# Optimization experiments

Measured on AMD Instinct MI355X. Metric: run time of the kernel, lower is better.

Reference implementation:

```python
import jax, jax.numpy as jnp
import numpy as np

SHIFT, REDUCE = 3, 2
B, L, E, H = 64, 512, 300, 256


def _make_transitions():
    # Left-branching valid parse: S S R S R S R ... (L shifts, L-1 reduces)
    T = 2 * L - 1
    tr = np.full(T, REDUCE, dtype=np.int64)
    tr[0] = SHIFT
    tr[1::2] = SHIFT
    return jnp.asarray(np.tile(tr[None, :], (B, 1)))


def setup_inputs() -> dict:
    key = jax.random.key(0)
    ks = jax.random.split(key, 5)
    s = 0.05
    return {
        "sentence": jax.random.normal(ks[0], (B, L, E), jnp.float32),
        "transitions": _make_transitions(),
        "W_word": jax.random.normal(ks[1], (E, 2 * H), jnp.float32) * s,
        "b_word": jnp.zeros((2 * H,), jnp.float32),
        "W_left": jax.random.normal(ks[2], (H, 5 * H), jnp.float32) * s,
        "W_right": jax.random.normal(ks[3], (H, 5 * H), jnp.float32) * s,
        "b_reduce": jnp.zeros((5 * H,), jnp.float32),
    }


def reference(sentence, transitions, W_word, b_word, W_left, W_right, b_reduce):
    Bsz, Ls, _ = sentence.shape
    Hs = W_left.shape[0]
    proj = sentence @ W_word + b_word                  # [B, L, 2H] (word projection; BN/dropout disabled)
    h_buf, c_buf = jnp.split(proj, 2, axis=2)          # buffers, each [B, L, H]
    T = transitions.shape[1]
    bidx = jnp.arange(Bsz)

    def step(carry, trans_t):
        sh, sc, ptr, bp = carry                        # thin stacks [B,T+2,H], pointers [B]
        shift = trans_t == SHIFT
        i1 = jnp.maximum(ptr - 1, 0)                   # right child (stack top)
        i2 = jnp.maximum(ptr - 2, 0)                   # left child
        hl, cl = sh[bidx, i2], sc[bidx, i2]
        hr, cr = sh[bidx, i1], sc[bidx, i1]
        g = hl @ W_left + hr @ W_right + b_reduce      # [B, 5H] TreeLSTM gates
        ig, flg, frg, og, ug = jnp.split(g, 5, axis=1)
        c_red = (jax.nn.sigmoid(flg) * cl + jax.nn.sigmoid(frg) * cr
                 + jax.nn.sigmoid(ig) * jnp.tanh(ug))
        h_red = jax.nn.sigmoid(og) * jnp.tanh(c_red)
        bsafe = jnp.minimum(bp, Ls - 1)
        val_h = jnp.where(shift[:, None], h_buf[bidx, bsafe], h_red)
        val_c = jnp.where(shift[:, None], c_buf[bidx, bsafe], c_red)
        pos = jnp.where(shift, ptr, i2)                # shift pushes at ptr; reduce writes at ptr-2
        sh = sh.at[bidx, pos].set(val_h)
        sc = sc.at[bidx, pos].set(val_c)
        ptr = ptr + jnp.where(shift, 1, -1)
        bp = bp + shift.astype(bp.dtype)
        return (sh, sc, ptr, bp), None

    sh0 = jnp.zeros((Bsz, T + 2, Hs), sentence.dtype)
    sc0 = jnp.zeros((Bsz, T + 2, Hs), sentence.dtype)
    ptr0 = jnp.zeros((Bsz,), jnp.int32)
    bp0 = jnp.zeros((Bsz,), jnp.int32)
    (sh, sc, ptr, _), _ = jax.lax.scan(
        step, (sh0, sc0, ptr0, bp0), jnp.swapaxes(transitions, 0, 1))
    return sh[bidx, jnp.maximum(ptr - 1, 0)]           # final stack top h: [B, H]
```

## Files before the change

### kernel.cpp

```cpp
#include <hip/hip_runtime.h>
#include <hip/hip_bf16.h>
#include <math.h>

#define BSZ   64
#define LSEQ  512
#define EDIM  300
#define HDIM  256
#define TLEN  1023
#define PROJW 512
#define GW    1280

#define NROW  8
#define NHID  8
#define RGBLK 32
#define NRG   8
#define NBLK  256
#define SLOTS 2

#define PROJ_N   (BSZ*LSEQ*PROJW)
#define STACKF   PROJ_N
#define STACK_N  (2*BSZ*SLOTS*2*HDIM)
#define FLAG_OFF (STACKF + STACK_N)
#define FLAGS_N  1024
#define ARR_OFF  (FLAG_OFF + FLAGS_N)
#define ARR_STRIDE 16

#define NODEBIT 0x80000000u
#define SENT    0xFFFFFFFFu
#define LROW    264
#define HRO     (NROW*LROW + 4)
#define RPITCH  328
#define RROW    41

__global__ void __launch_bounds__(256)
proj_gemm(const float* __restrict__ A, const float* __restrict__ W,
          const float* __restrict__ bias, float* __restrict__ out) {
    __shared__ float As[8][65];
    __shared__ float Bs[8][64];
    const int tid = threadIdx.x;
    const int tx = tid & 15, ty = tid >> 4;
    const int bm = blockIdx.y, bn = blockIdx.x;

    float acc[4][4] = {};
    const int e  = tid * 2;
    const int ar = e >> 3, ac = e & 7;
    const int br = e >> 6, bc = e & 63;

    for (int k0 = 0; k0 < EDIM; k0 += 8) {
        __syncthreads();
        {
            const float* Ap = A + (size_t)(bm * 64 + ar) * EDIM;
            int gk = k0 + ac;
            As[ac][ar]     = (gk     < EDIM) ? Ap[gk]     : 0.f;
            As[ac + 1][ar] = (gk + 1 < EDIM) ? Ap[gk + 1] : 0.f;
            int gkb = k0 + br;
            float w0 = 0.f, w1 = 0.f;
            if (gkb < EDIM) {
                const float* Wp = W + (size_t)gkb * PROJW + bn * 64;
                w0 = Wp[bc]; w1 = Wp[bc + 1];
            }
            Bs[br][bc] = w0; Bs[br][bc + 1] = w1;
        }
        __syncthreads();
        #pragma unroll
        for (int kk = 0; kk < 8; ++kk) {
            float a[4], b[4];
            #pragma unroll
            for (int i = 0; i < 4; ++i) a[i] = As[kk][ty * 4 + i];
            #pragma unroll
            for (int j = 0; j < 4; ++j) b[j] = Bs[kk][tx * 4 + j];
            #pragma unroll
            for (int i = 0; i < 4; ++i)
                #pragma unroll
                for (int j = 0; j < 4; ++j)
                    acc[i][j] += a[i] * b[j];
        }
    }
    #pragma unroll
    for (int i = 0; i < 4; ++i) {
        const int row  = bm * 64 + ty * 4 + i;
        const int col0 = bn * 64 + tx * 4;
        float* op = out + (size_t)row * PROJW + col0;
        #pragma unroll
        for (int j = 0; j < 4; ++j) op[j] = acc[i][j] + bias[col0 + j];
    }
}

__global__ void flags_kernel(const int* __restrict__ trans, int* __restrict__ flags) {
    const int t = blockIdx.x * 256 + threadIdx.x;
    if (t >= TLEN) return;
    int f = 0;
    for (int b = 0; b < BSZ; ++b) f |= (trans[(size_t)b * TLEN + t] != 3) ? 1 : 0;
    flags[t] = f;
}

__device__ __forceinline__ unsigned encodeH(short tag, int slot, int grow) {
    if (tag >= 0)  return (unsigned)(((size_t)grow * LSEQ + (int)tag) * PROJW);
    if (tag <= -3) return SENT;
    const int par = (tag == -2) ? 1 : 0;
    return NODEBIT | (unsigned)(STACKF + ((par * BSZ + grow) * SLOTS + slot) * (2 * HDIM));
}

__device__ __forceinline__ float cohLoad(const float* ws, unsigned off) {
    return __uint_as_float(__hip_atomic_load((const unsigned*)ws + off,
                          __ATOMIC_RELAXED, __HIP_MEMORY_SCOPE_AGENT));
}
__device__ __forceinline__ float2 cohLoad2(const float* ws, unsigned off) {
    unsigned long long v = __hip_atomic_load((const unsigned long long*)(ws + off),
                          __ATOMIC_RELAXED, __HIP_MEMORY_SCOPE_AGENT);
    union { unsigned long long u; float2 f; } cv; cv.u = v;
    return cv.f;
}
__device__ __forceinline__ void cohStore(float* ws, unsigned off, float v) {
    __hip_atomic_store((unsigned*)ws + off, __float_as_uint(v),
                       __ATOMIC_RELAXED, __HIP_MEMORY_SCOPE_AGENT);
}

__device__ __forceinline__ float loadC(const float* ws, unsigned oh, int gn) {
    if (oh == SENT) return 0.f;
    if (oh & NODEBIT) return cohLoad(ws, (oh & ~NODEBIT) + HDIM + gn);
    return ws[oh + HDIM + gn];
}

__device__ __forceinline__ int qswz(int Q, int row) {
    return Q ^ row ^ ((Q >> 3) & 7);
}

__device__ __forceinline__ void stage_rows(float* __restrict__ buf,
    const unsigned* __restrict__ desc, const int* __restrict__ isred,
    const float* __restrict__ ws, int srow, int sc, bool nodePhase) {
    if (!isred[srow]) return;
    const unsigned oh = desc[srow];
    if (!nodePhase) {
        if (oh == SENT) {
            const float4 z = make_float4(0.f, 0.f, 0.f, 0.f);
            #pragma unroll
            for (int j = 0; j < 2; ++j) {
                const int Q = sc + 32 * j;
                *(float4*)&buf[srow * LROW + 4 * qswz(Q, srow)] = z;
            }
        } else if (!(oh & NODEBIT)) {
            const float4* s = (const float4*)(ws + oh);
            #pragma unroll
            for (int j = 0; j < 2; ++j) {
                const int Q = sc + 32 * j;
                *(float4*)&buf[srow * LROW + 4 * qswz(Q, srow)] = s[Q];
            }
        }
    } else if (oh != SENT && (oh & NODEBIT)) {
        const unsigned base = oh & ~NODEBIT;
        #pragma unroll
        for (int j = 0; j < 2; ++j) {
            const int Q = sc + 32 * j;
            const float2 lo = cohLoad2(ws, base + 4 * Q);
            const float2 hi = cohLoad2(ws, base + 4 * Q + 2);
            *(float4*)&buf[srow * LROW + 4 * qswz(Q, srow)] = make_float4(lo.x, lo.y, hi.x, hi.y);
        }
    }
}

__global__ void __launch_bounds__(256, 1)
scan_coop(const int* __restrict__ trans,
          const float* __restrict__ Wl, const float* __restrict__ Wr,
          const float* __restrict__ bred,
          float* __restrict__ ws, float* __restrict__ out) {
    __shared__ __align__(16) float hbuf[HRO + NROW * LROW];
    __shared__ __align__(16) float red[16 * RPITCH];
    __shared__ unsigned tbits[NROW][32];
    __shared__ unsigned fbits[32];
    __shared__ short    tg[NROW][SLOTS];
    __shared__ unsigned d_hl[NROW], d_hr[NROW], d_wr[NROW], d_oh[NROW];
    __shared__ int      isred[NROW];

    const int tid   = threadIdx.x;
    const int rg    = blockIdx.x & 7;
    const int cs    = blockIdx.x >> 3;
    const int rbase = rg * NROW;
    const int n0    = cs * NHID;

    const int srow = tid >> 5, sc = tid & 31;
    const int colq = tid & 7;
    const int rh   = (tid >> 3) & 1;
    const int m    = (tid >> 4) & 1;
    const int w8   = tid >> 5;
    const int gn   = n0 + colq;

    const int* flags  = (const int*)(ws + FLAG_OFF);
    unsigned*  arr    = (unsigned*)(ws + ARR_OFF);
    unsigned*  myslot = &arr[(size_t)blockIdx.x * ARR_STRIDE];

    float4 w[8][5];
    {
        const float* src = (m == 0) ? Wl : Wr;
        const int kbase = w8 * 32;
        #pragma unroll
        for (int j = 0; j < 8; ++j) {
            const int k0 = kbase + j * 4;
            #pragma unroll
            for (int g = 0; g < 5; ++g) {
                w[j][g].x = src[(size_t)(k0 + 0) * GW + g * HDIM + gn];
                w[j][g].y = src[(size_t)(k0 + 1) * GW + g * HDIM + gn];
                w[j][g].z = src[(size_t)(k0 + 2) * GW + g * HDIM + gn];
                w[j][g].w = src[(size_t)(k0 + 3) * GW + g * HDIM + gn];
            }
        }
    }
    #pragma unroll
    for (int j = 0; j < 8; ++j)
        #pragma unroll
        for (int g = 0; g < 5; ++g)
            asm volatile("" : "+v"(w[j][g].x), "+v"(w[j][g].y),
                              "+v"(w[j][g].z), "+v"(w[j][g].w));

    if (tid < NROW * 32) {
        const int r2 = tid >> 5, wd = tid & 31;
        unsigned bits = 0;
        for (int j = 0; j < 32; ++j) {
            const int t = wd * 32 + j;
            if (t < TLEN && trans[(size_t)(rbase + r2) * TLEN + t] == 3) bits |= (1u << j);
        }
        tbits[r2][wd] = bits;
    }
    if (tid < 32) {
        unsigned bits = 0;
        for (int j = 0; j < 32; ++j) {
            const int t = tid * 32 + j;
            if (t < TLEN && flags[t]) bits |= (1u << j);
        }
        fbits[tid] = bits;
    }
    if (tid < NROW) {
        tg[tid][0] = -3; tg[tid][1] = -3;
        isred[tid] = 0;
    }

    float bv[5];
    #pragma unroll
    for (int g = 0; g < 5; ++g) bv[g] = bred[g * HDIM + gn];

    int ptr = 0, bp = 0;
    unsigned nbar = 0;
    __syncthreads();

    for (int t = 0; t < TLEN; ++t) {
        if (tid < NROW) {
            const int r = tid, grow = rbase + r;
            const int is_shift = (tbits[r][t >> 5] >> (t & 31)) & 1;
            if (is_shift) {
                int pos = ptr; if (pos < 0) pos = 0; if (pos > SLOTS - 1) pos = SLOTS - 1;
                tg[r][pos] = (short)min(bp, LSEQ - 1);
                ptr++; bp++;
                isred[r] = 0;
            } else {
                const int i1 = min(max(ptr - 1, 0), SLOTS - 1);
                const int i2 = min(max(ptr - 2, 0), SLOTS - 1);
                const short t1 = tg[r][i1], t2 = tg[r][i2];
                d_hl[r] = encodeH(t2, i2, grow);
                d_hr[r] = encodeH(t1, i1, grow);
                const int pnew = (t2 == -1) ? 1 : 0;
                d_wr[r] = (unsigned)(STACKF + ((pnew * BSZ + grow) * SLOTS + i2) * (2 * HDIM));
                tg[r][i2] = (short)(pnew ? -2 : -1);
                ptr--;
                isred[r] = 1;
            }
        }
        __syncthreads();

        if (!((fbits[t >> 5] >> (t & 31)) & 1)) continue;
        ++nbar;

        stage_rows(hbuf,       d_hl, isred, ws, srow, sc, false);
        stage_rows(hbuf + HRO, d_hr, isred, ws, srow, sc, false);

        if (tid < RGBLK) {
            const unsigned* slot = &arr[(size_t)(tid * NRG + rg) * ARR_STRIDE];
            while (__hip_atomic_load(slot, __ATOMIC_RELAXED, __HIP_MEMORY_SCOPE_AGENT) < nbar - 1)
                __builtin_amdgcn_s_sleep(1);
        }
        __syncthreads();

        stage_rows(hbuf,       d_hl, isred, ws, srow, sc, true);
        stage_rows(hbuf + HRO, d_hr, isred, ws, srow, sc, true);
        __syncthreads();

        float cl = 0.f, cr = 0.f;
        if (tid < 64) {
            const int orow = tid >> 3;
            if (isred[orow]) {
                cl = loadC(ws, d_hl[orow], gn);
                cr = loadC(ws, d_hr[orow], gn);
            }
        }

        float acc[4][5];
        #pragma unroll
        for (int r = 0; r < 4; ++r)
            #pragma unroll
            for (int g = 0; g < 5; ++g) acc[r][g] = 0.f;

        {
            const float* hb = hbuf + m * HRO;
            #pragma unroll
            for (int j = 0; j < 8; ++j) {
                const int kq = w8 * 8 + j;
                #pragma unroll
                for (int r = 0; r < 4; ++r) {
                    const int row = rh * 4 + r;
                    const float4 x = *(const float4*)&hb[row * LROW + 4 * qswz(kq, row)];
                    #pragma unroll
                    for (int g = 0; g < 5; ++g)
                        acc[r][g] += x.x * w[j][g].x + x.y * w[j][g].y
                                   + x.z * w[j][g].z + x.w * w[j][g].w;
                }
            }
        }

        {
            const int g16 = w8 * 2 + m;
            #pragma unroll
            for (int r = 0; r < 4; ++r) {
                const int row = rh * 4 + r;
                #pragma unroll
                for (int g = 0; g < 5; ++g)
                    red[g16 * RPITCH + row * RROW + colq * 5 + g] = acc[r][g];
            }
        }
        __syncthreads();

        if (tid < 64) {
            const int orow = tid >> 3;
            if (isred[orow]) {
                float s[5];
                #pragma unroll
                for (int g = 0; g < 5; ++g) s[g] = bv[g];
                #pragma unroll
                for (int q = 0; q < 16; ++q)
                    #pragma unroll
                    for (int g = 0; g < 5; ++g)
                        s[g] += red[q * RPITCH + orow * RROW + colq * 5 + g];
                const float si = 1.f / (1.f + expf(-s[0]));
                const float sl = 1.f / (1.f + expf(-s[1]));
                const float sr = 1.f / (1.f + expf(-s[2]));
                const float so = 1.f / (1.f + expf(-s[3]));
                const float c_red = sl * cl + sr * cr + si * tanhf(s[4]);
                const float h_red = so * tanhf(c_red);
                cohStore(ws, d_wr[orow] + gn, h_red);
                cohStore(ws, d_wr[orow] + HDIM + gn, c_red);
            }
            asm volatile("s_waitcnt vmcnt(0)" ::: "memory");
            if (tid == 0)
                __hip_atomic_store(myslot, nbar, __ATOMIC_RELAXED, __HIP_MEMORY_SCOPE_AGENT);
        }
    }

    if (tid < RGBLK) {
        const unsigned* slot = &arr[(size_t)(tid * NRG + rg) * ARR_STRIDE];
        while (__hip_atomic_load(slot, __ATOMIC_RELAXED, __HIP_MEMORY_SCOPE_AGENT) < nbar)
            __builtin_amdgcn_s_sleep(1);
    }
    __syncthreads();
    if (tid < NROW) {
        const int top = min(max(ptr - 1, 0), SLOTS - 1);
        d_oh[tid] = encodeH(tg[tid][top], top, rbase + tid);
    }
    __syncthreads();
    if (tid < 64) {
        const int orow = tid >> 3;
        const unsigned oh = d_oh[orow];
        float v;
        if (oh == SENT) v = 0.f;
        else if (oh & NODEBIT) v = cohLoad(ws, (oh & ~NODEBIT) + gn);
        else v = ws[oh + gn];
        out[(size_t)(rbase + orow) * HDIM + gn] = v;
    }
}

extern "C" void kernel_launch(void* const* d_in, const int* in_sizes, int n_in,
                              void* d_out, int out_size, void* d_ws, size_t ws_size,
                              hipStream_t stream) {
    const float* sentence    = (const float*)d_in[0];
    const int*   transitions = (const int*)  d_in[1];
    const float* W_word      = (const float*)d_in[2];
    const float* b_word      = (const float*)d_in[3];
    const float* W_left      = (const float*)d_in[4];
    const float* W_right     = (const float*)d_in[5];
    const float* b_reduce    = (const float*)d_in[6];
    float* out  = (float*)d_out;
    float* ws_f = (float*)d_ws;

    hipMemsetAsync((char*)d_ws + (size_t)ARR_OFF * 4, 0,
                   (size_t)NBLK * ARR_STRIDE * 4, stream);

    flags_kernel<<<(TLEN + 255) / 256, 256, 0, stream>>>(
        transitions, (int*)(ws_f + FLAG_OFF));

    dim3 g1(PROJW / 64, (BSZ * LSEQ) / 64);
    proj_gemm<<<g1, 256, 0, stream>>>(sentence, W_word, b_word, ws_f);

    scan_coop<<<NBLK, 256, 0, stream>>>(transitions, W_left, W_right, b_reduce,
                                        ws_f, out);
}
```

Before: 2.849 ms.

## Replace per-step block barrier with epoch-tagged h values and local c stack

Removes the per-step cross-block flag barrier. Each reduced h value is now stored as a 64-bit word whose upper half holds the step epoch, so consumers spin only on the exact data they need instead of on 32 producer block flags. Cell states c stay in shared memory, because each block owns its own hidden columns, so they no longer round-trip through global memory. The reduce-step flags are now derived in-kernel from the transition bits of the block's own 8 rows, which drops the flags kernel. This narrows synchronization to true data dependencies, at the cost of wider atomic loads and spin-polling per element.

```diff
diff --git a/kernel.cpp b/kernel.cpp
--- a/kernel.cpp
+++ b/kernel.cpp
@@ -12,18 +12,15 @@
 
 #define NROW  8
 #define NHID  8
-#define RGBLK 32
 #define NRG   8
 #define NBLK  256
 #define SLOTS 2
 
 #define PROJ_N   (BSZ*LSEQ*PROJW)
 #define STACKF   PROJ_N
-#define STACK_N  (2*BSZ*SLOTS*2*HDIM)
-#define FLAG_OFF (STACKF + STACK_N)
-#define FLAGS_N  1024
-#define ARR_OFF  (FLAG_OFF + FLAGS_N)
-#define ARR_STRIDE 16
+#define PAIRB    (STACKF/2)
+#define PAIR_N   (2*BSZ*SLOTS*HDIM)
+#define PAIR_CNT (2*BSZ*SLOTS*HDIM)
 
 #define NODEBIT 0x80000000u
 #define SENT    0xFFFFFFFFu
@@ -86,77 +83,8 @@
     }
 }
 
-__global__ void flags_kernel(const int* __restrict__ trans, int* __restrict__ flags) {
-    const int t = blockIdx.x * 256 + threadIdx.x;
-    if (t >= TLEN) return;
-    int f = 0;
-    for (int b = 0; b < BSZ; ++b) f |= (trans[(size_t)b * TLEN + t] != 3) ? 1 : 0;
-    flags[t] = f;
-}
-
-__device__ __forceinline__ unsigned encodeH(short tag, int slot, int grow) {
-    if (tag >= 0)  return (unsigned)(((size_t)grow * LSEQ + (int)tag) * PROJW);
-    if (tag <= -3) return SENT;
-    const int par = (tag == -2) ? 1 : 0;
-    return NODEBIT | (unsigned)(STACKF + ((par * BSZ + grow) * SLOTS + slot) * (2 * HDIM));
-}
-
-__device__ __forceinline__ float cohLoad(const float* ws, unsigned off) {
-    return __uint_as_float(__hip_atomic_load((const unsigned*)ws + off,
-                          __ATOMIC_RELAXED, __HIP_MEMORY_SCOPE_AGENT));
-}
-__device__ __forceinline__ float2 cohLoad2(const float* ws, unsigned off) {
-    unsigned long long v = __hip_atomic_load((const unsigned long long*)(ws + off),
-                          __ATOMIC_RELAXED, __HIP_MEMORY_SCOPE_AGENT);
-    union { unsigned long long u; float2 f; } cv; cv.u = v;
-    return cv.f;
-}
-__device__ __forceinline__ void cohStore(float* ws, unsigned off, float v) {
-    __hip_atomic_store((unsigned*)ws + off, __float_as_uint(v),
-                       __ATOMIC_RELAXED, __HIP_MEMORY_SCOPE_AGENT);
-}
-
-__device__ __forceinline__ float loadC(const float* ws, unsigned oh, int gn) {
-    if (oh == SENT) return 0.f;
-    if (oh & NODEBIT) return cohLoad(ws, (oh & ~NODEBIT) + HDIM + gn);
-    return ws[oh + HDIM + gn];
-}
-
 __device__ __forceinline__ int qswz(int Q, int row) {
     return Q ^ row ^ ((Q >> 3) & 7);
-}
-
-__device__ __forceinline__ void stage_rows(float* __restrict__ buf,
-    const unsigned* __restrict__ desc, const int* __restrict__ isred,
-    const float* __restrict__ ws, int srow, int sc, bool nodePhase) {
-    if (!isred[srow]) return;
-    const unsigned oh = desc[srow];
-    if (!nodePhase) {
-        if (oh == SENT) {
-            const float4 z = make_float4(0.f, 0.f, 0.f, 0.f);
-            #pragma unroll
-            for (int j = 0; j < 2; ++j) {
-                const int Q = sc + 32 * j;
-                *(float4*)&buf[srow * LROW + 4 * qswz(Q, srow)] = z;
-            }
-        } else if (!(oh & NODEBIT)) {
-            const float4* s = (const float4*)(ws + oh);
-            #pragma unroll
-            for (int j = 0; j < 2; ++j) {
-                const int Q = sc + 32 * j;
-                *(float4*)&buf[srow * LROW + 4 * qswz(Q, srow)] = s[Q];
-            }
-        }
-    } else if (oh != SENT && (oh & NODEBIT)) {
-        const unsigned base = oh & ~NODEBIT;
-        #pragma unroll
-        for (int j = 0; j < 2; ++j) {
-            const int Q = sc + 32 * j;
-            const float2 lo = cohLoad2(ws, base + 4 * Q);
-            const float2 hi = cohLoad2(ws, base + 4 * Q + 2);
-            *(float4*)&buf[srow * LROW + 4 * qswz(Q, srow)] = make_float4(lo.x, lo.y, hi.x, hi.y);
-        }
-    }
 }
 
 __global__ void __launch_bounds__(256, 1)
@@ -166,10 +94,15 @@
           float* __restrict__ ws, float* __restrict__ out) {
     __shared__ __align__(16) float hbuf[HRO + NROW * LROW];
     __shared__ __align__(16) float red[16 * RPITCH];
+    __shared__ float    cstk[2 * SLOTS * NROW * NHID];
     __shared__ unsigned tbits[NROW][32];
     __shared__ unsigned fbits[32];
     __shared__ short    tg[NROW][SLOTS];
-    __shared__ unsigned d_hl[NROW], d_hr[NROW], d_wr[NROW], d_oh[NROW];
+    __shared__ unsigned eps[NROW][SLOTS];
+    __shared__ unsigned d_hl[NROW], d_hr[NROW], d_wr[NROW];
+    __shared__ unsigned e_hl[NROW], e_hr[NROW];
+    __shared__ unsigned c_l[NROW], c_r[NROW], cw[NROW];
+    __shared__ unsigned d_oh[NROW], e_oh[NROW];
     __shared__ int      isred[NROW];
 
     const int tid   = threadIdx.x;
@@ -184,10 +117,9 @@
     const int m    = (tid >> 4) & 1;
     const int w8   = tid >> 5;
     const int gn   = n0 + colq;
-
-    const int* flags  = (const int*)(ws + FLAG_OFF);
-    unsigned*  arr    = (unsigned*)(ws + ARR_OFF);
-    unsigned*  myslot = &arr[(size_t)blockIdx.x * ARR_STRIDE];
+    const int orow = tid >> 3;
+
+    unsigned long long* p64 = (unsigned long long*)ws;
 
     float4 w[8][5];
     {
@@ -221,17 +153,18 @@
         }
         tbits[r2][wd] = bits;
     }
-    if (tid < 32) {
-        unsigned bits = 0;
-        for (int j = 0; j < 32; ++j) {
-            const int t = tid * 32 + j;
-            if (t < TLEN && flags[t]) bits |= (1u << j);
-        }
-        fbits[tid] = bits;
-    }
     if (tid < NROW) {
         tg[tid][0] = -3; tg[tid][1] = -3;
+        eps[tid][0] = 0; eps[tid][1] = 0;
         isred[tid] = 0;
+    }
+    __syncthreads();
+    if (tid < 32) {
+        unsigned fb = 0;
+        #pragma unroll
+        for (int r2 = 0; r2 < NROW; ++r2) fb |= ~tbits[r2][tid];
+        if (tid == 31) fb &= 0x7FFFFFFFu;
+        fbits[tid] = fb;
     }
 
     float bv[5];
@@ -243,6 +176,9 @@
     __syncthreads();
 
     for (int t = 0; t < TLEN; ++t) {
+        const int redstep = (fbits[t >> 5] >> (t & 31)) & 1;
+        if (redstep) ++nbar;
+
         if (tid < NROW) {
             const int r = tid, grow = rbase + r;
             const int is_shift = (tbits[r][t >> 5] >> (t & 31)) & 1;
@@ -255,10 +191,26 @@
                 const int i1 = min(max(ptr - 1, 0), SLOTS - 1);
                 const int i2 = min(max(ptr - 2, 0), SLOTS - 1);
                 const short t1 = tg[r][i1], t2 = tg[r][i2];
-                d_hl[r] = encodeH(t2, i2, grow);
-                d_hr[r] = encodeH(t1, i1, grow);
+                unsigned dl, el = 0, cdl;
+                if (t2 >= 0)       { dl = (unsigned)((grow * LSEQ + (int)t2) * PROJW); cdl = dl + HDIM; }
+                else if (t2 <= -3) { dl = SENT; cdl = SENT; }
+                else { const int par = (t2 == -2);
+                       dl = NODEBIT | (unsigned)(PAIRB + ((par * BSZ + grow) * SLOTS + i2) * HDIM);
+                       el = eps[r][i2];
+                       cdl = NODEBIT | (unsigned)(par * 2 + i2); }
+                unsigned dr, er = 0, cdr;
+                if (t1 >= 0)       { dr = (unsigned)((grow * LSEQ + (int)t1) * PROJW); cdr = dr + HDIM; }
+                else if (t1 <= -3) { dr = SENT; cdr = SENT; }
+                else { const int par = (t1 == -2);
+                       dr = NODEBIT | (unsigned)(PAIRB + ((par * BSZ + grow) * SLOTS + i1) * HDIM);
+                       er = eps[r][i1];
+                       cdr = NODEBIT | (unsigned)(par * 2 + i1); }
+                d_hl[r] = dl; e_hl[r] = el; c_l[r] = cdl;
+                d_hr[r] = dr; e_hr[r] = er; c_r[r] = cdr;
                 const int pnew = (t2 == -1) ? 1 : 0;
-                d_wr[r] = (unsigned)(STACKF + ((pnew * BSZ + grow) * SLOTS + i2) * (2 * HDIM));
+                d_wr[r] = (unsigned)(PAIRB + ((pnew * BSZ + grow) * SLOTS + i2) * HDIM);
+                cw[r]   = (unsigned)(pnew * 2 + i2);
+                eps[r][i2] = nbar;
                 tg[r][i2] = (short)(pnew ? -2 : -1);
                 ptr--;
                 isred[r] = 1;
@@ -266,30 +218,54 @@
         }
         __syncthreads();
 
-        if (!((fbits[t >> 5] >> (t & 31)) & 1)) continue;
-        ++nbar;
-
-        stage_rows(hbuf,       d_hl, isred, ws, srow, sc, false);
-        stage_rows(hbuf + HRO, d_hr, isred, ws, srow, sc, false);
-
-        if (tid < RGBLK) {
-            const unsigned* slot = &arr[(size_t)(tid * NRG + rg) * ARR_STRIDE];
-            while (__hip_atomic_load(slot, __ATOMIC_RELAXED, __HIP_MEMORY_SCOPE_AGENT) < nbar - 1)
-                __builtin_amdgcn_s_sleep(1);
-        }
-        __syncthreads();
-
-        stage_rows(hbuf,       d_hl, isred, ws, srow, sc, true);
-        stage_rows(hbuf + HRO, d_hr, isred, ws, srow, sc, true);
-        __syncthreads();
-
-        float cl = 0.f, cr = 0.f;
-        if (tid < 64) {
-            const int orow = tid >> 3;
-            if (isred[orow]) {
-                cl = loadC(ws, d_hl[orow], gn);
-                cr = loadC(ws, d_hr[orow], gn);
-            }
+        if (!redstep) continue;
+
+        if (isred[srow]) {
+            #pragma unroll
+            for (int buf = 0; buf < 2; ++buf) {
+                float* hb = hbuf + buf * HRO;
+                const unsigned oh = buf ? d_hr[srow] : d_hl[srow];
+                const unsigned ee = buf ? e_hr[srow] : e_hl[srow];
+                float h[8];
+                if (oh == SENT) {
+                    #pragma unroll
+                    for (int i = 0; i < 8; ++i) h[i] = 0.f;
+                } else if (!(oh & NODEBIT)) {
+                    const float4 a = *(const float4*)(ws + oh + sc * 8);
+                    const float4 b = *(const float4*)(ws + oh + sc * 8 + 4);
+                    h[0]=a.x; h[1]=a.y; h[2]=a.z; h[3]=a.w;
+                    h[4]=b.x; h[5]=b.y; h[6]=b.z; h[7]=b.w;
+                } else {
+                    const unsigned pb = (oh & ~NODEBIT) + sc * 8;
+                    unsigned long long v[8];
+                    for (;;) {
+                        #pragma unroll
+                        for (int i = 0; i < 8; ++i)
+                            v[i] = __hip_atomic_load(p64 + pb + i,
+                                     __ATOMIC_RELAXED, __HIP_MEMORY_SCOPE_AGENT);
+                        bool ok = true;
+                        #pragma unroll
+                        for (int i = 0; i < 8; ++i)
+                            ok &= ((unsigned)(v[i] >> 32) >= ee);
+                        if (ok) break;
+                        __builtin_amdgcn_s_sleep(1);
+                    }
+                    #pragma unroll
+                    for (int i = 0; i < 8; ++i) h[i] = __uint_as_float((unsigned)v[i]);
+                }
+                *(float4*)&hb[srow * LROW + 4 * qswz(2 * sc + 0, srow)] =
+                    make_float4(h[0], h[1], h[2], h[3]);
+                *(float4*)&hb[srow * LROW + 4 * qswz(2 * sc + 1, srow)] =
+                    make_float4(h[4], h[5], h[6], h[7]);
+            }
+        }
+        __syncthreads();
+
+        float clw = 0.f, crw = 0.f;
+        if (tid < 64 && isred[orow]) {
+            const unsigned cdl = c_l[orow], cdr = c_r[orow];
+            if (cdl != SENT && !(cdl & NODEBIT)) clw = ws[cdl + gn];
+            if (cdr != SENT && !(cdr & NODEBIT)) crw = ws[cdr + gn];
         }
 
         float acc[4][5];
@@ -297,7 +273,6 @@
         for (int r = 0; r < 4; ++r)
             #pragma unroll
             for (int g = 0; g < 5; ++g) acc[r][g] = 0.f;
-
         {
             const float* hb = hbuf + m * HRO;
             #pragma unroll
@@ -314,7 +289,6 @@
                 }
             }
         }
-
         {
             const int g16 = w8 * 2 + m;
             #pragma unroll
@@ -328,7 +302,6 @@
         __syncthreads();
 
         if (tid < 64) {
-            const int orow = tid >> 3;
             if (isred[orow]) {
                 float s[5];
                 #pragma unroll
@@ -338,39 +311,53 @@
                     #pragma unroll
                     for (int g = 0; g < 5; ++g)
                         s[g] += red[q * RPITCH + orow * RROW + colq * 5 + g];
+                const unsigned cdl = c_l[orow], cdr = c_r[orow];
+                const float cl = (cdl == SENT) ? 0.f :
+                    ((cdl & NODEBIT) ? cstk[((cdl & 3) * NROW + orow) * NHID + colq] : clw);
+                const float cr = (cdr == SENT) ? 0.f :
+                    ((cdr & NODEBIT) ? cstk[((cdr & 3) * NROW + orow) * NHID + colq] : crw);
                 const float si = 1.f / (1.f + expf(-s[0]));
                 const float sl = 1.f / (1.f + expf(-s[1]));
                 const float sr = 1.f / (1.f + expf(-s[2]));
                 const float so = 1.f / (1.f + expf(-s[3]));
                 const float c_red = sl * cl + sr * cr + si * tanhf(s[4]);
                 const float h_red = so * tanhf(c_red);
-                cohStore(ws, d_wr[orow] + gn, h_red);
-                cohStore(ws, d_wr[orow] + HDIM + gn, c_red);
-            }
-            asm volatile("s_waitcnt vmcnt(0)" ::: "memory");
-            if (tid == 0)
-                __hip_atomic_store(myslot, nbar, __ATOMIC_RELAXED, __HIP_MEMORY_SCOPE_AGENT);
-        }
-    }
-
-    if (tid < RGBLK) {
-        const unsigned* slot = &arr[(size_t)(tid * NRG + rg) * ARR_STRIDE];
-        while (__hip_atomic_load(slot, __ATOMIC_RELAXED, __HIP_MEMORY_SCOPE_AGENT) < nbar)
-            __builtin_amdgcn_s_sleep(1);
-    }
-    __syncthreads();
+                cstk[(cw[orow] * NROW + orow) * NHID + colq] = c_red;
+                const unsigned long long pv =
+                    ((unsigned long long)nbar << 32) | (unsigned long long)__float_as_uint(h_red);
+                __hip_atomic_store(p64 + d_wr[orow] + gn, pv,
+                                   __ATOMIC_RELAXED, __HIP_MEMORY_SCOPE_AGENT);
+            }
+        }
+    }
+
     if (tid < NROW) {
         const int top = min(max(ptr - 1, 0), SLOTS - 1);
-        d_oh[tid] = encodeH(tg[tid][top], top, rbase + tid);
+        const short tt = tg[tid][top];
+        const int grow = rbase + tid;
+        if (tt >= 0)       { d_oh[tid] = (unsigned)((grow * LSEQ + (int)tt) * PROJW); e_oh[tid] = 0; }
+        else if (tt <= -3) { d_oh[tid] = SENT; e_oh[tid] = 0; }
+        else { const int par = (tt == -2);
+               d_oh[tid] = NODEBIT | (unsigned)(PAIRB + ((par * BSZ + grow) * SLOTS + top) * HDIM);
+               e_oh[tid] = eps[tid][top]; }
     }
     __syncthreads();
     if (tid < 64) {
-        const int orow = tid >> 3;
         const unsigned oh = d_oh[orow];
         float v;
         if (oh == SENT) v = 0.f;
-        else if (oh & NODEBIT) v = cohLoad(ws, (oh & ~NODEBIT) + gn);
-        else v = ws[oh + gn];
+        else if (!(oh & NODEBIT)) v = ws[oh + gn];
+        else {
+            const unsigned pb = (oh & ~NODEBIT) + gn;
+            const unsigned ee = e_oh[orow];
+            unsigned long long pv;
+            for (;;) {
+                pv = __hip_atomic_load(p64 + pb, __ATOMIC_RELAXED, __HIP_MEMORY_SCOPE_AGENT);
+                if ((unsigned)(pv >> 32) >= ee) break;
+                __builtin_amdgcn_s_sleep(1);
+            }
+            v = __uint_as_float((unsigned)pv);
+        }
         out[(size_t)(rbase + orow) * HDIM + gn] = v;
     }
 }
@@ -388,11 +375,8 @@
     float* out  = (float*)d_out;
     float* ws_f = (float*)d_ws;
 
-    hipMemsetAsync((char*)d_ws + (size_t)ARR_OFF * 4, 0,
-                   (size_t)NBLK * ARR_STRIDE * 4, stream);
-
-    flags_kernel<<<(TLEN + 255) / 256, 256, 0, stream>>>(
-        transitions, (int*)(ws_f + FLAG_OFF));
+    hipMemsetAsync((char*)d_ws + (size_t)STACKF * 4, 0,
+                   (size_t)PAIR_CNT * 8, stream);
 
     dim3 g1(PROJW / 64, (BSZ * LSEQ) / 64);
     proj_gemm<<<g1, 256, 0, stream>>>(sentence, W_word, b_word, ws_f);
```

Result: no change. 2.818 ms (-1.1%).
